# Kernel tuning notes

Hardware: AMD Instinct MI355X
Metric: run time of the kernel (lower is better)

Reference implementation:

```python
import jax, jax.numpy as jnp
import numpy as np

N_NODES = 50000
N_EDGES = 800000
N_GRAPHS = 1000
F_IN = 128
HID = 64


def setup_inputs() -> dict:
    key = jax.random.key(0)
    ks = jax.random.split(key, 10)
    x = jax.random.normal(ks[0], (N_NODES, F_IN), dtype=jnp.float32)
    edge_index = jax.random.randint(ks[1], (2, N_EDGES), 0, N_NODES, dtype=jnp.int32)
    batch = jnp.sort(jax.random.randint(ks[2], (N_NODES,), 0, N_GRAPHS, dtype=jnp.int32))
    # GCNConv weights (glorot-ish scale) and biases
    W1 = jax.random.normal(ks[3], (F_IN, HID), dtype=jnp.float32) / np.sqrt(F_IN)
    b1 = jnp.zeros((HID,), dtype=jnp.float32)
    W2 = jax.random.normal(ks[4], (HID, HID), dtype=jnp.float32) / np.sqrt(HID)
    b2 = jnp.zeros((HID,), dtype=jnp.float32)
    Wl = jax.random.normal(ks[5], (HID, 1), dtype=jnp.float32) / np.sqrt(HID)
    bl = jnp.zeros((1,), dtype=jnp.float32)
    return {"x": x, "W1": W1, "b1": b1, "W2": W2, "b2": b2,
            "Wl": Wl, "bl": bl, "edge_index": edge_index, "batch": batch}


def reference(x, W1, b1, W2, b2, Wl, bl, edge_index, batch):
    N = x.shape[0]
    src, dst = edge_index[0], edge_index[1]
    # GCN symmetric normalization with self-loops: deg = 1 + in-degree
    deg = jnp.ones((N,), x.dtype).at[dst].add(jnp.float32(1.0))
    dis = jax.lax.rsqrt(deg)                       # deg^{-1/2}
    enorm = dis[src] * dis[dst]                    # [E] edge norm
    snorm = dis * dis                              # [N] self-loop norm

    def conv(h, W, b):
        h = h @ W                                  # [N, H]
        agg = jax.ops.segment_sum(h[src] * enorm[:, None], dst, num_segments=N)
        return agg + h * snorm[:, None] + b

    h = jax.nn.relu(conv(x, W1, b1))
    for _ in range(4):
        h = jax.nn.relu(conv(h, W2, b2))

    # global mean pool over graphs
    counts = jax.ops.segment_sum(jnp.ones((N,), h.dtype), batch, num_segments=N_GRAPHS)
    pooled = jax.ops.segment_sum(h, batch, num_segments=N_GRAPHS)
    pooled = pooled / jnp.maximum(counts, 1.0)[:, None]
    # dropout is identity in eval mode
    return pooled @ Wl + bl                        # [G, 1]
```

## Files before the change

### kernel.cpp

```cpp
#include <hip/hip_runtime.h>
#include <hip/hip_fp16.h>

#define N_NODES 50000
#define N_EDGES 800000
#define N_GRAPHS 1000
#define F_IN 128
#define HID 64
#define NBUCK 196
#define BCAP 5120

typedef _Float16 half8 __attribute__((ext_vector_type(8)));
typedef float f32x4v __attribute__((ext_vector_type(4)));

__device__ __forceinline__ int wave_incl_scan_i(int v, int lane) {
  #pragma unroll
  for (int off = 1; off < 64; off <<= 1) {
    int t = __shfl_up(v, off, 64);
    if (lane >= off) v += t;
  }
  return v;
}

__global__ __launch_bounds__(1024) void k_bucket(const int* __restrict__ src,
                                                 const int* __restrict__ dst,
                                                 int* __restrict__ bucket_cnt,
                                                 int2* __restrict__ region) {
  __shared__ int bcnt[NBUCK];
  __shared__ int lbase[NBUCK];
  __shared__ int gpos[NBUCK];
  __shared__ int2 stage[4096];
  int tid = threadIdx.x;
  if (tid < NBUCK) bcnt[tid] = 0;
  __syncthreads();
  int e0 = blockIdx.x * 4096;
  int2 rec0, rec1, rec2, rec3;
  int bk0 = -1, bk1 = -1, bk2 = -1, bk3 = -1;
  int rk0 = 0, rk1 = 0, rk2 = 0, rk3 = 0;
#define LOADA(i) { int e = e0 + tid + i * 1024;                                  \
    if (e < N_EDGES) { rec##i.x = src[e]; rec##i.y = dst[e];                     \
      bk##i = rec##i.y >> 8; rk##i = atomicAdd(&bcnt[bk##i], 1); } }
  LOADA(0) LOADA(1) LOADA(2) LOADA(3)
#undef LOADA
  __syncthreads();
  if (tid < 64) {
    int v0 = (tid * 4 + 0 < NBUCK) ? bcnt[tid * 4 + 0] : 0;
    int v1 = (tid * 4 + 1 < NBUCK) ? bcnt[tid * 4 + 1] : 0;
    int v2 = (tid * 4 + 2 < NBUCK) ? bcnt[tid * 4 + 2] : 0;
    int v3 = (tid * 4 + 3 < NBUCK) ? bcnt[tid * 4 + 3] : 0;
    int s = v0 + v1 + v2 + v3;
    int excl = wave_incl_scan_i(s, tid) - s;
    if (tid * 4 + 0 < NBUCK) lbase[tid * 4 + 0] = excl; excl += v0;
    if (tid * 4 + 1 < NBUCK) lbase[tid * 4 + 1] = excl; excl += v1;
    if (tid * 4 + 2 < NBUCK) lbase[tid * 4 + 2] = excl; excl += v2;
    if (tid * 4 + 3 < NBUCK) lbase[tid * 4 + 3] = excl;
  }
  __syncthreads();
  if (tid < NBUCK && bcnt[tid] > 0) gpos[tid] = atomicAdd(&bucket_cnt[tid], bcnt[tid]);
  if (bk0 >= 0) stage[lbase[bk0] + rk0] = rec0;
  if (bk1 >= 0) stage[lbase[bk1] + rk1] = rec1;
  if (bk2 >= 0) stage[lbase[bk2] + rk2] = rec2;
  if (bk3 >= 0) stage[lbase[bk3] + rk3] = rec3;
  __syncthreads();
  int total = lbase[NBUCK - 1] + bcnt[NBUCK - 1];
  for (int j = tid; j < total; j += 1024) {
    int2 r = stage[j];
    int b = r.y >> 8;
    int k = gpos[b] + (j - lbase[b]);
    if (k < BCAP) region[b * BCAP + k] = r;
  }
}

__global__ void k_bscan(const int* __restrict__ bucket_cnt,
                        int* __restrict__ bucket_base, int* __restrict__ offs) {
  int lane = threadIdx.x;
  int v0 = (lane * 4 + 0 < NBUCK) ? bucket_cnt[lane * 4 + 0] : 0;
  int v1 = (lane * 4 + 1 < NBUCK) ? bucket_cnt[lane * 4 + 1] : 0;
  int v2 = (lane * 4 + 2 < NBUCK) ? bucket_cnt[lane * 4 + 2] : 0;
  int v3 = (lane * 4 + 3 < NBUCK) ? bucket_cnt[lane * 4 + 3] : 0;
  int s = v0 + v1 + v2 + v3;
  int excl = wave_incl_scan_i(s, lane) - s;
  if (lane * 4 + 0 < NBUCK) bucket_base[lane * 4 + 0] = excl; excl += v0;
  if (lane * 4 + 1 < NBUCK) bucket_base[lane * 4 + 1] = excl; excl += v1;
  if (lane * 4 + 2 < NBUCK) bucket_base[lane * 4 + 2] = excl; excl += v2;
  if (lane * 4 + 3 < NBUCK) bucket_base[lane * 4 + 3] = excl;
  if (lane == 0) offs[N_NODES] = N_EDGES;
}

__global__ __launch_bounds__(1024) void k_csr(const int2* __restrict__ region,
                                              const int* __restrict__ bucket_cnt,
                                              const int* __restrict__ bucket_base,
                                              int* __restrict__ offs,
                                              float* __restrict__ dis,
                                              int* __restrict__ esrc) {
  __shared__ int hist[256];
  __shared__ int base[256];
  __shared__ int stage[BCAP];
  int b = blockIdx.x, tid = threadIdx.x;
  int cnt = bucket_cnt[b]; if (cnt > BCAP) cnt = BCAP;
  int bbase = bucket_base[b];
  if (tid < 256) hist[tid] = 0;
  __syncthreads();
  int rec0, rec1, rec2, rec3, rec4;
  int ln0 = -1, ln1 = -1, ln2 = -1, ln3 = -1, ln4 = -1;
  int rk0 = 0, rk1 = 0, rk2 = 0, rk3 = 0, rk4 = 0;
#define LOADB(i) { int j = tid + i * 1024;                                        \
    if (j < cnt) { int2 r = region[b * BCAP + j]; rec##i = r.x;                   \
      ln##i = r.y & 255; rk##i = atomicAdd(&hist[ln##i], 1); } }
  LOADB(0) LOADB(1) LOADB(2) LOADB(3) LOADB(4)
#undef LOADB
  __syncthreads();
  if (tid < 64) {
    int v0 = hist[tid * 4 + 0], v1 = hist[tid * 4 + 1];
    int v2 = hist[tid * 4 + 2], v3 = hist[tid * 4 + 3];
    int s = v0 + v1 + v2 + v3;
    int excl = wave_incl_scan_i(s, tid) - s;
    base[tid * 4 + 0] = excl; excl += v0;
    base[tid * 4 + 1] = excl; excl += v1;
    base[tid * 4 + 2] = excl; excl += v2;
    base[tid * 4 + 3] = excl;
  }
  __syncthreads();
  int node = b * 256 + tid;
  if (tid < 256 && node < N_NODES) {
    offs[node] = bbase + base[tid];
    dis[node] = rsqrtf(1.0f + (float)hist[tid]);
  }
  if (ln0 >= 0) stage[base[ln0] + rk0] = rec0;
  if (ln1 >= 0) stage[base[ln1] + rk1] = rec1;
  if (ln2 >= 0) stage[base[ln2] + rk2] = rec2;
  if (ln3 >= 0) stage[base[ln3] + rk3] = rec3;
  if (ln4 >= 0) stage[base[ln4] + rk4] = rec4;
  __syncthreads();
  for (int j = tid; j < cnt; j += 1024) esrc[bbase + j] = stage[j];
}

__device__ __forceinline__ void acc8_fp16(float* acc, uint4 u) {
  float2 f;
  f = __half22float2(*(__half2*)&u.x); acc[0] += f.x; acc[1] += f.y;
  f = __half22float2(*(__half2*)&u.y); acc[2] += f.x; acc[3] += f.y;
  f = __half22float2(*(__half2*)&u.z); acc[4] += f.x; acc[5] += f.y;
  f = __half22float2(*(__half2*)&u.w); acc[6] += f.x; acc[7] += f.y;
}

__global__ __launch_bounds__(256) void k_gemm1_mfma(const float* __restrict__ X,
                                                    const float* __restrict__ W,
                                                    const float* __restrict__ dis,
                                                    __half* __restrict__ T) {
  __shared__ __half wt[128 * 64];
  const int tid = threadIdx.x;
  for (int i = tid; i < 8192; i += 256) {
    int k = i >> 6, col = i & 63;
    int boff = (col << 8) + ((k << 1) ^ ((col & 7) << 4));
    *(__half*)((char*)wt + boff) = __float2half(W[k * 64 + col]);
  }
  __syncthreads();

  const int w = tid >> 6, l = tid & 63;
  const int row0 = blockIdx.x * 64 + w * 16;
  const int arow = row0 + (l & 15);
  const int koff = (l >> 4) << 3;

  half8 a[4];
  #pragma unroll
  for (int s = 0; s < 4; ++s) {
    half8 av = {};
    if (arow < N_NODES) {
      float4 f0 = *(const float4*)&X[arow * 128 + s * 32 + koff];
      float4 f1 = *(const float4*)&X[arow * 128 + s * 32 + koff + 4];
      av[0] = (_Float16)f0.x; av[1] = (_Float16)f0.y;
      av[2] = (_Float16)f0.z; av[3] = (_Float16)f0.w;
      av[4] = (_Float16)f1.x; av[5] = (_Float16)f1.y;
      av[6] = (_Float16)f1.z; av[7] = (_Float16)f1.w;
    }
    a[s] = av;
  }
  f32x4v acc[4] = {{0.f,0.f,0.f,0.f},{0.f,0.f,0.f,0.f},
                   {0.f,0.f,0.f,0.f},{0.f,0.f,0.f,0.f}};
  #pragma unroll
  for (int t = 0; t < 4; ++t) {
    int col = (t << 4) + (l & 15);
    #pragma unroll
    for (int s = 0; s < 4; ++s) {
      int kk = s * 32 + koff;
      half8 b = *(const half8*)((const char*)wt +
                 ((col << 8) + ((kk << 1) ^ ((col & 7) << 4))));
      acc[t] = __builtin_amdgcn_mfma_f32_16x16x32_f16(a[s], b, acc[t], 0, 0, 0);
    }
  }
  #pragma unroll
  for (int r = 0; r < 4; ++r) {
    int row = row0 + ((l >> 4) << 2) + r;
    if (row < N_NODES) {
      float dn = dis[row];
      #pragma unroll
      for (int t = 0; t < 4; ++t)
        T[row * 64 + (t << 4) + (l & 15)] = __float2half(acc[t][r] * dn);
    }
  }
}

__global__ __launch_bounds__(256) void k_gg(const __half* __restrict__ T,
                                            const int* __restrict__ offs,
                                            const int* __restrict__ esrc,
                                            const float* __restrict__ dis,
                                            const float* __restrict__ bias,
                                            const float* __restrict__ W,
                                            __half* __restrict__ Tout) {
  __shared__ __half wt[64 * 64];
  __shared__ __half hs[32 * 64];
  const int tid = threadIdx.x;
  for (int i = tid; i < 4096; i += 256) {
    int k = i >> 6, col = i & 63;
    int boff = (col << 7) + ((k << 1) ^ ((col & 7) << 4));
    *(__half*)((char*)wt + boff) = __float2half(W[k * 64 + col]);
  }

  const int n0 = blockIdx.x * 32;
  const int nloc = tid >> 3;
  const int n = n0 + nloc;
  const int l8 = (tid & 7) << 3;
  uint4 hu = make_uint4(0u, 0u, 0u, 0u);
  if (n < N_NODES) {
    int e0 = offs[n], e1 = offs[n + 1];
    float acc[8] = {};
    acc8_fp16(acc, *(const uint4*)&T[n * 64 + l8]);
    int e = e0;
    for (; e + 8 <= e1; e += 8) {
      int s0 = esrc[e+0], s1 = esrc[e+1], s2 = esrc[e+2], s3 = esrc[e+3];
      int s4 = esrc[e+4], s5 = esrc[e+5], s6 = esrc[e+6], s7 = esrc[e+7];
      uint4 u0 = *(const uint4*)&T[s0 * 64 + l8];
      uint4 u1 = *(const uint4*)&T[s1 * 64 + l8];
      uint4 u2 = *(const uint4*)&T[s2 * 64 + l8];
      uint4 u3 = *(const uint4*)&T[s3 * 64 + l8];
      uint4 u4 = *(const uint4*)&T[s4 * 64 + l8];
      uint4 u5 = *(const uint4*)&T[s5 * 64 + l8];
      uint4 u6 = *(const uint4*)&T[s6 * 64 + l8];
      uint4 u7 = *(const uint4*)&T[s7 * 64 + l8];
      acc8_fp16(acc, u0); acc8_fp16(acc, u1); acc8_fp16(acc, u2); acc8_fp16(acc, u3);
      acc8_fp16(acc, u4); acc8_fp16(acc, u5); acc8_fp16(acc, u6); acc8_fp16(acc, u7);
    }
    for (; e + 4 <= e1; e += 4) {
      int s0 = esrc[e+0], s1 = esrc[e+1], s2 = esrc[e+2], s3 = esrc[e+3];
      uint4 u0 = *(const uint4*)&T[s0 * 64 + l8];
      uint4 u1 = *(const uint4*)&T[s1 * 64 + l8];
      uint4 u2 = *(const uint4*)&T[s2 * 64 + l8];
      uint4 u3 = *(const uint4*)&T[s3 * 64 + l8];
      acc8_fp16(acc, u0); acc8_fp16(acc, u1); acc8_fp16(acc, u2); acc8_fp16(acc, u3);
    }
    for (; e < e1; ++e) {
      acc8_fp16(acc, *(const uint4*)&T[esrc[e] * 64 + l8]);
    }
    float dn = dis[n];
    float4 b0 = *(const float4*)&bias[l8];
    float4 b1 = *(const float4*)&bias[l8 + 4];
    __half2 h0 = __floats2half2_rn(fmaxf(fmaf(dn, acc[0], b0.x), 0.f),
                                   fmaxf(fmaf(dn, acc[1], b0.y), 0.f));
    __half2 h1 = __floats2half2_rn(fmaxf(fmaf(dn, acc[2], b0.z), 0.f),
                                   fmaxf(fmaf(dn, acc[3], b0.w), 0.f));
    __half2 h2 = __floats2half2_rn(fmaxf(fmaf(dn, acc[4], b1.x), 0.f),
                                   fmaxf(fmaf(dn, acc[5], b1.y), 0.f));
    __half2 h3 = __floats2half2_rn(fmaxf(fmaf(dn, acc[6], b1.z), 0.f),
                                   fmaxf(fmaf(dn, acc[7], b1.w), 0.f));
    hu = make_uint4(*(unsigned*)&h0, *(unsigned*)&h1,
                    *(unsigned*)&h2, *(unsigned*)&h3);
  }
  *(uint4*)((char*)hs + ((nloc << 7) + ((l8 << 1) ^ ((nloc & 7) << 4)))) = hu;
  __syncthreads();

  const int w = tid >> 6, l = tid & 63;
  const int rt = (w >> 1) << 4;
  const int ct0 = (w & 1) << 1;
  const int arowl = rt + (l & 15);
  const int koff = (l >> 4) << 3;
  half8 a0 = *(const half8*)((const char*)hs +
              ((arowl << 7) + ((koff << 1) ^ ((arowl & 7) << 4))));
  half8 a1 = *(const half8*)((const char*)hs +
              ((arowl << 7) + (((koff + 32) << 1) ^ ((arowl & 7) << 4))));
  f32x4v acc2[2] = {{0.f,0.f,0.f,0.f},{0.f,0.f,0.f,0.f}};
  #pragma unroll
  for (int t = 0; t < 2; ++t) {
    int col = ((ct0 + t) << 4) + (l & 15);
    half8 b0 = *(const half8*)((const char*)wt +
                ((col << 7) + ((koff << 1) ^ ((col & 7) << 4))));
    half8 b1 = *(const half8*)((const char*)wt +
                ((col << 7) + (((koff + 32) << 1) ^ ((col & 7) << 4))));
    acc2[t] = __builtin_amdgcn_mfma_f32_16x16x32_f16(a0, b0, acc2[t], 0, 0, 0);
    acc2[t] = __builtin_amdgcn_mfma_f32_16x16x32_f16(a1, b1, acc2[t], 0, 0, 0);
  }
  #pragma unroll
  for (int r = 0; r < 4; ++r) {
    int row = n0 + rt + ((l >> 4) << 2) + r;
    if (row < N_NODES) {
      float dn = dis[row];
      #pragma unroll
      for (int t = 0; t < 2; ++t)
        Tout[row * 64 + ((ct0 + t) << 4) + (l & 15)] = __float2half(acc2[t][r] * dn);
    }
  }
}

__global__ __launch_bounds__(256) void k_final(const __half* __restrict__ T,
                                               const int* __restrict__ offs,
                                               const int* __restrict__ esrc,
                                               const float* __restrict__ dis,
                                               const float* __restrict__ bias,
                                               const float* __restrict__ Wl,
                                               float* __restrict__ pern) {
  int tid = threadIdx.x;
  int n = blockIdx.x * 32 + (tid >> 3);
  int l8 = (tid & 7) << 3;
  if (n >= N_NODES) return;
  int e0 = offs[n], e1 = offs[n + 1];
  float acc[8] = {};
  acc8_fp16(acc, *(const uint4*)&T[n * 64 + l8]);
  int e = e0;
  for (; e + 8 <= e1; e += 8) {
    int s0 = esrc[e+0], s1 = esrc[e+1], s2 = esrc[e+2], s3 = esrc[e+3];
    int s4 = esrc[e+4], s5 = esrc[e+5], s6 = esrc[e+6], s7 = esrc[e+7];
    uint4 u0 = *(const uint4*)&T[s0 * 64 + l8];
    uint4 u1 = *(const uint4*)&T[s1 * 64 + l8];
    uint4 u2 = *(const uint4*)&T[s2 * 64 + l8];
    uint4 u3 = *(const uint4*)&T[s3 * 64 + l8];
    uint4 u4 = *(const uint4*)&T[s4 * 64 + l8];
    uint4 u5 = *(const uint4*)&T[s5 * 64 + l8];
    uint4 u6 = *(const uint4*)&T[s6 * 64 + l8];
    uint4 u7 = *(const uint4*)&T[s7 * 64 + l8];
    acc8_fp16(acc, u0); acc8_fp16(acc, u1); acc8_fp16(acc, u2); acc8_fp16(acc, u3);
    acc8_fp16(acc, u4); acc8_fp16(acc, u5); acc8_fp16(acc, u6); acc8_fp16(acc, u7);
  }
  for (; e + 4 <= e1; e += 4) {
    int s0 = esrc[e+0], s1 = esrc[e+1], s2 = esrc[e+2], s3 = esrc[e+3];
    uint4 u0 = *(const uint4*)&T[s0 * 64 + l8];
    uint4 u1 = *(const uint4*)&T[s1 * 64 + l8];
    uint4 u2 = *(const uint4*)&T[s2 * 64 + l8];
    uint4 u3 = *(const uint4*)&T[s3 * 64 + l8];
    acc8_fp16(acc, u0); acc8_fp16(acc, u1); acc8_fp16(acc, u2); acc8_fp16(acc, u3);
  }
  for (; e < e1; ++e) {
    acc8_fp16(acc, *(const uint4*)&T[esrc[e] * 64 + l8]);
  }
  float dn = dis[n];
  float4 b0 = *(const float4*)&bias[l8];
  float4 b1 = *(const float4*)&bias[l8 + 4];
  float4 w0 = *(const float4*)&Wl[l8];
  float4 w1 = *(const float4*)&Wl[l8 + 4];
  float s = fmaxf(fmaf(dn, acc[0], b0.x), 0.f) * w0.x
          + fmaxf(fmaf(dn, acc[1], b0.y), 0.f) * w0.y
          + fmaxf(fmaf(dn, acc[2], b0.z), 0.f) * w0.z
          + fmaxf(fmaf(dn, acc[3], b0.w), 0.f) * w0.w
          + fmaxf(fmaf(dn, acc[4], b1.x), 0.f) * w1.x
          + fmaxf(fmaf(dn, acc[5], b1.y), 0.f) * w1.y
          + fmaxf(fmaf(dn, acc[6], b1.z), 0.f) * w1.z
          + fmaxf(fmaf(dn, acc[7], b1.w), 0.f) * w1.w;
  s += __shfl_xor(s, 1, 64);
  s += __shfl_xor(s, 2, 64);
  s += __shfl_xor(s, 4, 64);
  if ((tid & 7) == 0) pern[n] = s;
}

__global__ __launch_bounds__(64) void k_pool2(const float* __restrict__ pern,
                                              const int* __restrict__ batch,
                                              const float* __restrict__ bl,
                                              float* __restrict__ out) {
  int g = blockIdx.x;
  int lane = threadIdx.x;
  int lo = 0, hi = N_NODES;
  while (lo < hi) { int mid = (lo + hi) >> 1; if (batch[mid] < g) lo = mid + 1; else hi = mid; }
  int start = lo;
  hi = N_NODES;
  while (lo < hi) { int mid = (lo + hi) >> 1; if (batch[mid] < g + 1) lo = mid + 1; else hi = mid; }
  int end = lo;
  float acc = 0.f;
  for (int nn = start + lane; nn < end; nn += 64) acc += pern[nn];
  #pragma unroll
  for (int off = 32; off; off >>= 1) acc += __shfl_down(acc, off, 64);
  if (lane == 0) {
    float cntf = (float)(end - start);
    out[g] = acc / fmaxf(cntf, 1.0f) + bl[0];
  }
}

extern "C" void kernel_launch(void* const* d_in, const int* in_sizes, int n_in,
                              void* d_out, int out_size, void* d_ws, size_t ws_size,
                              hipStream_t stream) {
  const float* x    = (const float*)d_in[0];
  const float* W1   = (const float*)d_in[1];
  const float* b1   = (const float*)d_in[2];
  const float* W2   = (const float*)d_in[3];
  const float* b2   = (const float*)d_in[4];
  const float* Wl   = (const float*)d_in[5];
  const float* bl   = (const float*)d_in[6];
  const int*   eidx = (const int*)d_in[7];
  const int*   batch= (const int*)d_in[8];
  const int* e_src = eidx;
  const int* e_dst = eidx + N_EDGES;
  float* out = (float*)d_out;

  char* w = (char*)d_ws;
  size_t o = 0;
  auto alloc = [&](size_t bytes) { void* p = w + o; o += (bytes + 255) & ~(size_t)255; return p; };
  float*  dis    = (float*) alloc(N_NODES * 4);
  int*    offs   = (int*)   alloc((N_NODES + 1) * 4);
  int*    esrc   = (int*)   alloc((size_t)N_EDGES * 4);
  int*    bcnt   = (int*)   alloc(NBUCK * 4);
  int*    bbase  = (int*)   alloc(NBUCK * 4);
  int2*   region = (int2*)  alloc((size_t)NBUCK * BCAP * 8);
  __half* bufT   = (__half*)alloc((size_t)N_NODES * HID * 2);
  __half* bufU   = (__half*)alloc((size_t)N_NODES * HID * 2);
  float*  pern   = (float*) alloc(N_NODES * 4);

  const int NBG = (N_NODES + 63) / 64;
  const int NGA = (N_NODES + 31) / 32;

  (void)hipMemsetAsync(bcnt, 0, NBUCK * 4, stream);
  k_bucket<<<(N_EDGES + 4095) / 4096, 1024, 0, stream>>>(e_src, e_dst, bcnt, region);
  k_bscan <<<1, 64, 0, stream>>>(bcnt, bbase, offs);
  k_csr   <<<NBUCK, 1024, 0, stream>>>(region, bcnt, bbase, offs, dis, esrc);

  k_gemm1_mfma<<<NBG, 256, 0, stream>>>(x, W1, dis, bufT);
  k_gg  <<<NGA, 256, 0, stream>>>(bufT, offs, esrc, dis, b1, W2, bufU);
  k_gg  <<<NGA, 256, 0, stream>>>(bufU, offs, esrc, dis, b2, W2, bufT);
  k_gg  <<<NGA, 256, 0, stream>>>(bufT, offs, esrc, dis, b2, W2, bufU);
  k_gg  <<<NGA, 256, 0, stream>>>(bufU, offs, esrc, dis, b2, W2, bufT);
  k_final<<<NGA, 256, 0, stream>>>(bufT, offs, esrc, dis, b2, Wl, pern);
  k_pool2<<<N_GRAPHS, 64, 0, stream>>>(pern, batch, bl, out);
}
```

Baseline: 140.9 us.

## Split LDS histogram atomics, fold bucket scan into CSR, precompute W2 fp16

The bucket and CSR kernels now spread their shared-memory histogram atomics over four per-wavegroup copies to cut contention, and the separate single-wave bucket-scan kernel is removed by recomputing the scan inside each CSR block. W2 is converted and swizzled to fp16 once in a new prep kernel rather than inside every k_gg block. k_gg grows to 512 threads covering 64 nodes per block. The trade is redundant per-block scans and a larger shared footprint, and k_gg's unseen middle section must handle 64 nodes correctly.

Measured after the change: 143.8 us. +2.0%, slower.

```diff
diff --git a/kernel.cpp b/kernel.cpp
--- a/kernel.cpp
+++ b/kernel.cpp
@@ -21,16 +21,27 @@
   return v;
 }
 
+__global__ void k_prep(const float* __restrict__ W, __half* __restrict__ wt16) {
+  int i = blockIdx.x * 256 + threadIdx.x;
+  if (i < 4096) {
+    int k = i >> 6, col = i & 63;
+    int boff = (col << 7) + ((k << 1) ^ ((col & 7) << 4));
+    *(__half*)((char*)wt16 + boff) = __float2half(W[k * 64 + col]);
+  }
+}
+
 __global__ __launch_bounds__(1024) void k_bucket(const int* __restrict__ src,
                                                  const int* __restrict__ dst,
                                                  int* __restrict__ bucket_cnt,
                                                  int2* __restrict__ region) {
-  __shared__ int bcnt[NBUCK];
-  __shared__ int lbase[NBUCK];
+  __shared__ int cnt4[4][NBUCK];
+  __shared__ int gbase[NBUCK];
   __shared__ int gpos[NBUCK];
+  __shared__ int tot[NBUCK];
   __shared__ int2 stage[4096];
-  int tid = threadIdx.x;
-  if (tid < NBUCK) bcnt[tid] = 0;
+  const int tid = threadIdx.x;
+  const int copy = tid >> 8;
+  for (int i = tid; i < 4 * NBUCK; i += 1024) ((int*)cnt4)[i] = 0;
   __syncthreads();
   int e0 = blockIdx.x * 4096;
   int2 rec0, rec1, rec2, rec3;
@@ -38,80 +49,93 @@
   int rk0 = 0, rk1 = 0, rk2 = 0, rk3 = 0;
 #define LOADA(i) { int e = e0 + tid + i * 1024;                                  \
     if (e < N_EDGES) { rec##i.x = src[e]; rec##i.y = dst[e];                     \
-      bk##i = rec##i.y >> 8; rk##i = atomicAdd(&bcnt[bk##i], 1); } }
+      bk##i = rec##i.y >> 8; rk##i = atomicAdd(&cnt4[copy][bk##i], 1); } }
   LOADA(0) LOADA(1) LOADA(2) LOADA(3)
 #undef LOADA
   __syncthreads();
+  if (tid < NBUCK)
+    tot[tid] = cnt4[0][tid] + cnt4[1][tid] + cnt4[2][tid] + cnt4[3][tid];
+  __syncthreads();
   if (tid < 64) {
-    int v0 = (tid * 4 + 0 < NBUCK) ? bcnt[tid * 4 + 0] : 0;
-    int v1 = (tid * 4 + 1 < NBUCK) ? bcnt[tid * 4 + 1] : 0;
-    int v2 = (tid * 4 + 2 < NBUCK) ? bcnt[tid * 4 + 2] : 0;
-    int v3 = (tid * 4 + 3 < NBUCK) ? bcnt[tid * 4 + 3] : 0;
+    int v0 = (tid * 4 + 0 < NBUCK) ? tot[tid * 4 + 0] : 0;
+    int v1 = (tid * 4 + 1 < NBUCK) ? tot[tid * 4 + 1] : 0;
+    int v2 = (tid * 4 + 2 < NBUCK) ? tot[tid * 4 + 2] : 0;
+    int v3 = (tid * 4 + 3 < NBUCK) ? tot[tid * 4 + 3] : 0;
     int s = v0 + v1 + v2 + v3;
     int excl = wave_incl_scan_i(s, tid) - s;
-    if (tid * 4 + 0 < NBUCK) lbase[tid * 4 + 0] = excl; excl += v0;
-    if (tid * 4 + 1 < NBUCK) lbase[tid * 4 + 1] = excl; excl += v1;
-    if (tid * 4 + 2 < NBUCK) lbase[tid * 4 + 2] = excl; excl += v2;
-    if (tid * 4 + 3 < NBUCK) lbase[tid * 4 + 3] = excl;
-  }
-  __syncthreads();
-  if (tid < NBUCK && bcnt[tid] > 0) gpos[tid] = atomicAdd(&bucket_cnt[tid], bcnt[tid]);
-  if (bk0 >= 0) stage[lbase[bk0] + rk0] = rec0;
-  if (bk1 >= 0) stage[lbase[bk1] + rk1] = rec1;
-  if (bk2 >= 0) stage[lbase[bk2] + rk2] = rec2;
-  if (bk3 >= 0) stage[lbase[bk3] + rk3] = rec3;
-  __syncthreads();
-  int total = lbase[NBUCK - 1] + bcnt[NBUCK - 1];
+    if (tid * 4 + 0 < NBUCK) gbase[tid * 4 + 0] = excl; excl += v0;
+    if (tid * 4 + 1 < NBUCK) gbase[tid * 4 + 1] = excl; excl += v1;
+    if (tid * 4 + 2 < NBUCK) gbase[tid * 4 + 2] = excl; excl += v2;
+    if (tid * 4 + 3 < NBUCK) gbase[tid * 4 + 3] = excl;
+  }
+  __syncthreads();
+  if (tid < NBUCK) {
+    int b0 = gbase[tid];
+    int c0 = cnt4[0][tid], c1 = cnt4[1][tid], c2 = cnt4[2][tid];
+    cnt4[0][tid] = b0;
+    cnt4[1][tid] = b0 + c0;
+    cnt4[2][tid] = b0 + c0 + c1;
+    cnt4[3][tid] = b0 + c0 + c1 + c2;
+    int t = tot[tid];
+    if (t > 0) gpos[tid] = atomicAdd(&bucket_cnt[tid], t);
+  }
+  __syncthreads();
+  if (bk0 >= 0) stage[cnt4[copy][bk0] + rk0] = rec0;
+  if (bk1 >= 0) stage[cnt4[copy][bk1] + rk1] = rec1;
+  if (bk2 >= 0) stage[cnt4[copy][bk2] + rk2] = rec2;
+  if (bk3 >= 0) stage[cnt4[copy][bk3] + rk3] = rec3;
+  __syncthreads();
+  int total = gbase[NBUCK - 1] + tot[NBUCK - 1];
   for (int j = tid; j < total; j += 1024) {
     int2 r = stage[j];
     int b = r.y >> 8;
-    int k = gpos[b] + (j - lbase[b]);
+    int k = gpos[b] + (j - gbase[b]);
     if (k < BCAP) region[b * BCAP + k] = r;
   }
-}
-
-__global__ void k_bscan(const int* __restrict__ bucket_cnt,
-                        int* __restrict__ bucket_base, int* __restrict__ offs) {
-  int lane = threadIdx.x;
-  int v0 = (lane * 4 + 0 < NBUCK) ? bucket_cnt[lane * 4 + 0] : 0;
-  int v1 = (lane * 4 + 1 < NBUCK) ? bucket_cnt[lane * 4 + 1] : 0;
-  int v2 = (lane * 4 + 2 < NBUCK) ? bucket_cnt[lane * 4 + 2] : 0;
-  int v3 = (lane * 4 + 3 < NBUCK) ? bucket_cnt[lane * 4 + 3] : 0;
-  int s = v0 + v1 + v2 + v3;
-  int excl = wave_incl_scan_i(s, lane) - s;
-  if (lane * 4 + 0 < NBUCK) bucket_base[lane * 4 + 0] = excl; excl += v0;
-  if (lane * 4 + 1 < NBUCK) bucket_base[lane * 4 + 1] = excl; excl += v1;
-  if (lane * 4 + 2 < NBUCK) bucket_base[lane * 4 + 2] = excl; excl += v2;
-  if (lane * 4 + 3 < NBUCK) bucket_base[lane * 4 + 3] = excl;
-  if (lane == 0) offs[N_NODES] = N_EDGES;
 }
 
 __global__ __launch_bounds__(1024) void k_csr(const int2* __restrict__ region,
                                               const int* __restrict__ bucket_cnt,
-                                              const int* __restrict__ bucket_base,
                                               int* __restrict__ offs,
                                               float* __restrict__ dis,
                                               int* __restrict__ esrc) {
-  __shared__ int hist[256];
+  __shared__ int sbase[NBUCK];
+  __shared__ int h4[4][256];
+  __shared__ int tot[256];
   __shared__ int base[256];
   __shared__ int stage[BCAP];
-  int b = blockIdx.x, tid = threadIdx.x;
+  const int b = blockIdx.x, tid = threadIdx.x;
+  const int copy = tid >> 8;
+  for (int i = tid; i < 1024; i += 1024) ((int*)h4)[i] = 0;
+  if (tid < 64) {
+    int v0 = (tid * 4 + 0 < NBUCK) ? bucket_cnt[tid * 4 + 0] : 0;
+    int v1 = (tid * 4 + 1 < NBUCK) ? bucket_cnt[tid * 4 + 1] : 0;
+    int v2 = (tid * 4 + 2 < NBUCK) ? bucket_cnt[tid * 4 + 2] : 0;
+    int v3 = (tid * 4 + 3 < NBUCK) ? bucket_cnt[tid * 4 + 3] : 0;
+    int s = v0 + v1 + v2 + v3;
+    int excl = wave_incl_scan_i(s, tid) - s;
+    if (tid * 4 + 0 < NBUCK) sbase[tid * 4 + 0] = excl; excl += v0;
+    if (tid * 4 + 1 < NBUCK) sbase[tid * 4 + 1] = excl; excl += v1;
+    if (tid * 4 + 2 < NBUCK) sbase[tid * 4 + 2] = excl; excl += v2;
+    if (tid * 4 + 3 < NBUCK) sbase[tid * 4 + 3] = excl;
+  }
+  __syncthreads();
   int cnt = bucket_cnt[b]; if (cnt > BCAP) cnt = BCAP;
-  int bbase = bucket_base[b];
-  if (tid < 256) hist[tid] = 0;
-  __syncthreads();
+  const int bbase = sbase[b];
   int rec0, rec1, rec2, rec3, rec4;
   int ln0 = -1, ln1 = -1, ln2 = -1, ln3 = -1, ln4 = -1;
   int rk0 = 0, rk1 = 0, rk2 = 0, rk3 = 0, rk4 = 0;
 #define LOADB(i) { int j = tid + i * 1024;                                        \
     if (j < cnt) { int2 r = region[b * BCAP + j]; rec##i = r.x;                   \
-      ln##i = r.y & 255; rk##i = atomicAdd(&hist[ln##i], 1); } }
+      ln##i = r.y & 255; rk##i = atomicAdd(&h4[copy][ln##i], 1); } }
   LOADB(0) LOADB(1) LOADB(2) LOADB(3) LOADB(4)
 #undef LOADB
   __syncthreads();
+  if (tid < 256) tot[tid] = h4[0][tid] + h4[1][tid] + h4[2][tid] + h4[3][tid];
+  __syncthreads();
   if (tid < 64) {
-    int v0 = hist[tid * 4 + 0], v1 = hist[tid * 4 + 1];
-    int v2 = hist[tid * 4 + 2], v3 = hist[tid * 4 + 3];
+    int v0 = tot[tid * 4 + 0], v1 = tot[tid * 4 + 1];
+    int v2 = tot[tid * 4 + 2], v3 = tot[tid * 4 + 3];
     int s = v0 + v1 + v2 + v3;
     int excl = wave_incl_scan_i(s, tid) - s;
     base[tid * 4 + 0] = excl; excl += v0;
@@ -120,16 +144,26 @@
     base[tid * 4 + 3] = excl;
   }
   __syncthreads();
-  int node = b * 256 + tid;
-  if (tid < 256 && node < N_NODES) {
-    offs[node] = bbase + base[tid];
-    dis[node] = rsqrtf(1.0f + (float)hist[tid]);
-  }
-  if (ln0 >= 0) stage[base[ln0] + rk0] = rec0;
-  if (ln1 >= 0) stage[base[ln1] + rk1] = rec1;
-  if (ln2 >= 0) stage[base[ln2] + rk2] = rec2;
-  if (ln3 >= 0) stage[base[ln3] + rk3] = rec3;
-  if (ln4 >= 0) stage[base[ln4] + rk4] = rec4;
+  if (tid < 256) {
+    int node = b * 256 + tid;
+    if (node < N_NODES) {
+      offs[node] = bbase + base[tid];
+      dis[node] = rsqrtf(1.0f + (float)tot[tid]);
+    }
+    int b0 = base[tid];
+    int c0 = h4[0][tid], c1 = h4[1][tid], c2 = h4[2][tid];
+    h4[0][tid] = b0;
+    h4[1][tid] = b0 + c0;
+    h4[2][tid] = b0 + c0 + c1;
+    h4[3][tid] = b0 + c0 + c1 + c2;
+  }
+  if (b == 0 && tid == 0) offs[N_NODES] = N_EDGES;
+  __syncthreads();
+  if (ln0 >= 0) stage[h4[copy][ln0] + rk0] = rec0;
+  if (ln1 >= 0) stage[h4[copy][ln1] + rk1] = rec1;
+  if (ln2 >= 0) stage[h4[copy][ln2] + rk2] = rec2;
+  if (ln3 >= 0) stage[h4[copy][ln3] + rk3] = rec3;
+  if (ln4 >= 0) stage[h4[copy][ln4] + rk4] = rec4;
   __syncthreads();
   for (int j = tid; j < cnt; j += 1024) esrc[bbase + j] = stage[j];
 }
@@ -199,23 +233,19 @@
   }
 }
 
-__global__ __launch_bounds__(256) void k_gg(const __half* __restrict__ T,
+__global__ __launch_bounds__(512) void k_gg(const __half* __restrict__ T,
                                             const int* __restrict__ offs,
                                             const int* __restrict__ esrc,
                                             const float* __restrict__ dis,
                                             const float* __restrict__ bias,
-                                            const float* __restrict__ W,
+                                            const __half* __restrict__ wt16,
                                             __half* __restrict__ Tout) {
   __shared__ __half wt[64 * 64];
-  __shared__ __half hs[32 * 64];
+  __shared__ __half hs[64 * 64];
   const int tid = threadIdx.x;
-  for (int i = tid; i < 4096; i += 256) {
-    int k = i >> 6, col = i & 63;
-    int boff = (col << 7) + ((k << 1) ^ ((col & 7) << 4));
-    *(__half*)((char*)wt + boff) = __float2half(W[k * 64 + col]);
-  }
-
-  const int n0 = blockIdx.x * 32;
+  ((uint4*)wt)[tid] = ((const uint4*)wt16)[tid];
+
+  const int n0 = blockIdx.x * 64;
   const int nloc = tid >> 3;
   const int n = n0 + nloc;
   const int l8 = (tid & 7) << 3;
@@ -403,25 +433,26 @@
   int*    offs   = (int*)   alloc((N_NODES + 1) * 4);
   int*    esrc   = (int*)   alloc((size_t)N_EDGES * 4);
   int*    bcnt   = (int*)   alloc(NBUCK * 4);
-  int*    bbase  = (int*)   alloc(NBUCK * 4);
   int2*   region = (int2*)  alloc((size_t)NBUCK * BCAP * 8);
+  __half* wt16   = (__half*)alloc(4096 * 2);
   __half* bufT   = (__half*)alloc((size_t)N_NODES * HID * 2);
   __half* bufU   = (__half*)alloc((size_t)N_NODES * HID * 2);
   float*  pern   = (float*) alloc(N_NODES * 4);
 
   const int NBG = (N_NODES + 63) / 64;
+  const int NGG = (N_NODES + 63) / 64;
   const int NGA = (N_NODES + 31) / 32;
 
   (void)hipMemsetAsync(bcnt, 0, NBUCK * 4, stream);
+  k_prep  <<<16, 256, 0, stream>>>(W2, wt16);
   k_bucket<<<(N_EDGES + 4095) / 4096, 1024, 0, stream>>>(e_src, e_dst, bcnt, region);
-  k_bscan <<<1, 64, 0, stream>>>(bcnt, bbase, offs);
-  k_csr   <<<NBUCK, 1024, 0, stream>>>(region, bcnt, bbase, offs, dis, esrc);
+  k_csr   <<<NBUCK, 1024, 0, stream>>>(region, bcnt, offs, dis, esrc);
 
   k_gemm1_mfma<<<NBG, 256, 0, stream>>>(x, W1, dis, bufT);
-  k_gg  <<<NGA, 256, 0, stream>>>(bufT, offs, esrc, dis, b1, W2, bufU);
-  k_gg  <<<NGA, 256, 0, stream>>>(bufU, offs, esrc, dis, b2, W2, bufT);
-  k_gg  <<<NGA, 256, 0, stream>>>(bufT, offs, esrc, dis, b2, W2, bufU);
-  k_gg  <<<NGA, 256, 0, stream>>>(bufU, offs, esrc, dis, b2, W2, bufT);
+  k_gg  <<<NGG, 512, 0, stream>>>(bufT, offs, esrc, dis, b1, wt16, bufU);
+  k_gg  <<<NGG, 512, 0, stream>>>(bufU, offs, esrc, dis, b2, wt16, bufT);
+  k_gg  <<<NGG, 512, 0, stream>>>(bufT, offs, esrc, dis, b2, wt16, bufU);
+  k_gg  <<<NGG, 512, 0, stream>>>(bufU, offs, esrc, dis, b2, wt16, bufT);
   k_final<<<NGA, 256, 0, stream>>>(bufT, offs, esrc, dis, b2, Wl, pern);
   k_pool2<<<N_GRAPHS, 64, 0, stream>>>(pern, batch, bl, out);
 }
```
